# Performance work log

Measured on AMD Instinct MI355X. Metric: run time of the kernel, lower is better.

The kernel has to match this reference:

```python
import jax, jax.numpy as jnp
import numpy as np


def setup_inputs() -> dict:
    key = jax.random.key(0)
    k1, k2 = jax.random.split(key)
    B, S, D_IN, D_OUT = 4, 8192, 768, 768
    x = jax.random.normal(k1, (B, S, D_IN), dtype=jnp.float32)
    # kaiming_normal_(mode='fan_out', nonlinearity='linear') -> std = 1/sqrt(fan_out)
    weight = jax.random.normal(k2, (D_OUT, D_IN), dtype=jnp.float32) * (1.0 / jnp.sqrt(D_OUT))
    return {"x": x, "weight": weight}


def reference(x, weight):
    # Binarize weights with sign (0 -> 0, matching torch.sign), then F.linear:
    # out[..., o] = sum_i x[..., i] * sign(W)[o, i]
    w_bin = jnp.sign(weight)
    return jnp.einsum('bsi,oi->bso', x, w_bin)
```

## Files before the change

### kernel.cpp

```cpp
#include <hip/hip_runtime.h>
#include <hip/hip_bf16.h>

using f32x4 = __attribute__((ext_vector_type(4))) float;
using s16x8 = __attribute__((ext_vector_type(8))) short;

constexpr int KDIM = 768;
constexpr int NDIM = 768;
constexpr int BM = 128;
constexpr int BN = 128;
constexpr int BK = 32;
constexpr int NBN = NDIM / BN;
constexpr int NT = KDIM / BK;

__device__ __forceinline__ unsigned short f2bf(float f) {
    __bf16 h = (__bf16)f;
    return __builtin_bit_cast(unsigned short, h);
}

__device__ __forceinline__ short sgnbf(float w) {
    unsigned u = __builtin_bit_cast(unsigned, w);
    return (w != 0.f) ? (short)(unsigned short)(0x3F80u | ((u >> 16) & 0x8000u))
                      : (short)0;
}

__device__ __forceinline__ s16x8 cvt8(float4 u, float4 v) {
    s16x8 c;
    c[0] = (short)f2bf(u.x); c[1] = (short)f2bf(u.y);
    c[2] = (short)f2bf(u.z); c[3] = (short)f2bf(u.w);
    c[4] = (short)f2bf(v.x); c[5] = (short)f2bf(v.y);
    c[6] = (short)f2bf(v.z); c[7] = (short)f2bf(v.w);
    return c;
}

__global__ void binarize_w(const float* __restrict__ W, unsigned short* __restrict__ Wf) {
    const int g = blockIdx.x * 256 + threadIdx.x;
    const int lane = g & 63;
    const int grp  = g >> 6;
    const int n16l = grp & 7;
    const int bkt  = grp >> 3;
    const int bn   = bkt % NBN;
    const int kt   = bkt / NBN;
    const int col  = bn * 128 + n16l * 16 + (lane & 15);
    const int k0   = kt * 32 + (lane >> 4) * 8;
    const float* src = W + (size_t)col * KDIM + k0;
    s16x8 r;
    #pragma unroll
    for (int j = 0; j < 8; ++j) r[j] = sgnbf(src[j]);
    *(s16x8*)(Wf + (size_t)g * 8) = r;
}

#define BAR_NODRAIN() do {                                        \
    asm volatile("s_waitcnt lgkmcnt(0)" ::: "memory");            \
    __builtin_amdgcn_s_barrier();                                 \
    asm volatile("" ::: "memory");                                \
} while (0)

__device__ __forceinline__ int swzs(int s) { return s ^ (((s >> 4) & 3) << 2); }

template<bool PRE>
__global__ __launch_bounds__(256, 3)
void binlin_mfma(const float* __restrict__ X, const float* __restrict__ W,
                 const unsigned short* __restrict__ Wf, float* __restrict__ Out) {
    __shared__ __align__(16) unsigned short As[2][512 * 8];

    const int bid = blockIdx.x;
    const int cpx = gridDim.x >> 3;
    const int swz = (bid & 7) * cpx + (bid >> 3);
    const int bm = swz / NBN;
    const int bn = swz - bm * NBN;

    const int t    = threadIdx.x;
    const int lane = t & 63;
    const int wid  = t >> 6;
    const int wm   = (wid >> 1) * 64;
    const int wn   = (wid & 1) * 64;
    const int wm16 = (wid >> 1) * 4;
    const int wn16 = (wid & 1) * 4;

    const float* Xb = X + (size_t)bm * BM * KDIM;

    const int r   = t >> 2;
    const int c8  = (t & 3) * 8;
    const float* Abase = Xb + (size_t)r * KDIM + c8;
    const int sA1 = swzs((r >> 4) * 64 + (r & 15) + 16 * (t & 3));
    const int sA2 = swzs((r >> 4) * 64 + (r & 15) + 16 * (t & 3) + 256);

    auto loadA = [&](int kt, float4 a[4]) {
        const float* p = Abase + kt * BK;
        a[0] = *(const float4*)p;
        a[1] = *(const float4*)(p + 4);
        a[2] = *(const float4*)(p + (size_t)64 * KDIM);
        a[3] = *(const float4*)(p + (size_t)64 * KDIM + 4);
    };
    auto writeA = [&](int buf, float4 a[4]) {
        *(s16x8*)&As[buf][(size_t)sA1 * 8] = cvt8(a[0], a[1]);
        *(s16x8*)&As[buf][(size_t)sA2 * 8] = cvt8(a[2], a[3]);
    };
    auto loadB = [&](int kt, s16x8 b[4]) {
        if constexpr (PRE) {
            const unsigned short* q =
                Wf + ((size_t)(kt * NBN + bn) * 512 + wn16 * 64 + lane) * 8;
            #pragma unroll
            for (int n = 0; n < 4; ++n)
                b[n] = *(const s16x8*)(q + (size_t)n * 64 * 8);
        } else {
            #pragma unroll
            for (int n = 0; n < 4; ++n) {
                const int col = bn * 128 + (wn16 + n) * 16 + (lane & 15);
                const int k0  = kt * 32 + (lane >> 4) * 8;
                const float* wp = W + (size_t)col * KDIM + k0;
                float4 u = *(const float4*)wp;
                float4 v = *(const float4*)(wp + 4);
                s16x8 c;
                c[0] = sgnbf(u.x); c[1] = sgnbf(u.y); c[2] = sgnbf(u.z); c[3] = sgnbf(u.w);
                c[4] = sgnbf(v.x); c[5] = sgnbf(v.y); c[6] = sgnbf(v.z); c[7] = sgnbf(v.w);
                b[n] = c;
            }
        }
    };

    f32x4 acc[4][4] = {};
    float4 A0[4], A1[4];
    s16x8 B0[4], B1[4];

    loadA(0, A0);
    loadA(1, A1);
    loadB(0, B0);
    writeA(0, A0);
    BAR_NODRAIN();

    #pragma unroll
    for (int kt = 0; kt < NT; ++kt) {
        const int c = kt & 1;
        float4 (&AL)[4] = c ? A1 : A0;
        float4 (&AW)[4] = c ? A0 : A1;
        s16x8 (&BC)[4]  = c ? B1 : B0;
        s16x8 (&BL)[4]  = c ? B0 : B1;

        if (kt + 2 < NT) loadA(kt + 2, AL);
        if (kt + 1 < NT) loadB(kt + 1, BL);

        s16x8 af[4];
        #pragma unroll
        for (int m = 0; m < 4; ++m)
            af[m] = *(const s16x8*)&As[c][(size_t)swzs((wm16 + m) * 64 + lane) * 8];

        #pragma unroll
        for (int m = 0; m < 4; ++m)
            #pragma unroll
            for (int n = 0; n < 4; ++n)
                acc[m][n] = __builtin_amdgcn_mfma_f32_16x16x32_bf16(
                    af[m], BC[n], acc[m][n], 0, 0, 0);

        if (kt + 1 < NT) {
            writeA(c ^ 1, AW);
            BAR_NODRAIN();
        }
    }

    float* Ob = Out + (size_t)(bm * BM) * NDIM + bn * BN;
    const int lr = lane & 15;
    #pragma unroll
    for (int m = 0; m < 4; ++m) {
        const int row0 = wm + m * 16 + (lane >> 4) * 4;
        #pragma unroll
        for (int n = 0; n < 4; ++n) {
            const int col = wn + n * 16 + lr;
            #pragma unroll
            for (int rr = 0; rr < 4; ++rr)
                Ob[(size_t)(row0 + rr) * NDIM + col] = acc[m][n][rr];
        }
    }
}

extern "C" void kernel_launch(void* const* d_in, const int* in_sizes, int n_in,
                              void* d_out, int out_size, void* d_ws, size_t ws_size,
                              hipStream_t stream) {
    const float* X = (const float*)d_in[0];
    const float* W = (const float*)d_in[1];
    float* Out = (float*)d_out;
    const int M = in_sizes[0] / KDIM;
    const int grid = (M / BM) * NBN;
    const size_t need = (size_t)NDIM * KDIM * sizeof(unsigned short);

    if (ws_size >= need) {
        unsigned short* Wf = (unsigned short*)d_ws;
        binarize_w<<<(NT * NBN * 8 * 64) / 256, 256, 0, stream>>>(W, Wf);
        binlin_mfma<true><<<grid, 256, 0, stream>>>(X, W, Wf, Out);
    } else {
        binlin_mfma<false><<<grid, 256, 0, stream>>>(X, W, nullptr, Out);
    }
}
```

Before: 63.19 us.

## Enlarge tiles to 128x256x64 with 8 waves and phased barrier-interleaved MFMA schedule

Changes the block tile to BN=256, BK=64 with 512 threads (8 waves), and restructures the main loop into four phases per K step. Each phase interleaves the global loads and LDS writes with MFMA bursts, separated by barriers and s_setprio. The aim is to increase reuse per block, halve the number of K iterations, and overlap memory traffic with matrix work. The costs are more barriers per step, the loss of the LDS swizzle (risking bank conflicts), and lower occupancy from the larger register and LDS footprint.

```diff
diff --git a/kernel.cpp b/kernel.cpp
--- a/kernel.cpp
+++ b/kernel.cpp
@@ -7,8 +7,8 @@
 constexpr int KDIM = 768;
 constexpr int NDIM = 768;
 constexpr int BM = 128;
-constexpr int BN = 128;
-constexpr int BK = 32;
+constexpr int BN = 256;
+constexpr int BK = 64;
 constexpr int NBN = NDIM / BN;
 constexpr int NT = KDIM / BK;
 
@@ -34,14 +34,16 @@
 
 __global__ void binarize_w(const float* __restrict__ W, unsigned short* __restrict__ Wf) {
     const int g = blockIdx.x * 256 + threadIdx.x;
-    const int lane = g & 63;
-    const int grp  = g >> 6;
-    const int n16l = grp & 7;
-    const int bkt  = grp >> 3;
-    const int bn   = bkt % NBN;
-    const int kt   = bkt / NBN;
-    const int col  = bn * 128 + n16l * 16 + (lane & 15);
-    const int k0   = kt * 32 + (lane >> 4) * 8;
+    const int lane  = g & 63;
+    const int sg    = g >> 6;
+    const int srow  = sg & 31;
+    const int chunk = sg >> 5;
+    const int bn = chunk % NBN;
+    const int kt = chunk / NBN;
+    const int kk  = srow >> 4;
+    const int n16 = srow & 15;
+    const int col = bn * 256 + n16 * 16 + (lane & 15);
+    const int k0  = kt * 64 + kk * 32 + (lane >> 4) * 8;
     const float* src = W + (size_t)col * KDIM + k0;
     s16x8 r;
     #pragma unroll
@@ -49,19 +51,37 @@
     *(s16x8*)(Wf + (size_t)g * 8) = r;
 }
 
-#define BAR_NODRAIN() do {                                        \
-    asm volatile("s_waitcnt lgkmcnt(0)" ::: "memory");            \
-    __builtin_amdgcn_s_barrier();                                 \
-    asm volatile("" ::: "memory");                                \
+#define PHASE(C, KK, MB, BARR, ...) do {                                       \
+    s16x8 af0_ = *(const s16x8*)&As[C][(size_t)(((KK)*8 + wr4 + (MB)) * 64 + lane) * 8];       \
+    s16x8 af1_ = *(const s16x8*)&As[C][(size_t)(((KK)*8 + wr4 + (MB) + 1) * 64 + lane) * 8];   \
+    __VA_ARGS__;                                                               \
+    __builtin_amdgcn_s_barrier();                                              \
+    __builtin_amdgcn_s_setprio(1);                                             \
+    _Pragma("unroll")                                                          \
+    for (int n_ = 0; n_ < 4; ++n_) {                                           \
+        acc[MB][n_]     = __builtin_amdgcn_mfma_f32_16x16x32_bf16(af0_, BARR[KK][n_], acc[MB][n_], 0, 0, 0);       \
+        acc[(MB)+1][n_] = __builtin_amdgcn_mfma_f32_16x16x32_bf16(af1_, BARR[KK][n_], acc[(MB)+1][n_], 0, 0, 0);   \
+    }                                                                          \
+    __builtin_amdgcn_s_setprio(0);                                             \
+    __builtin_amdgcn_s_barrier();                                              \
 } while (0)
 
-__device__ __forceinline__ int swzs(int s) { return s ^ (((s >> 4) & 3) << 2); }
+#define KSTEP(C, BCUR, BNXT, KT, PF) do {                                      \
+    PHASE(C, 0, 0, BCUR, { if (PF) loadA((KT) + 1, aR); });                    \
+    PHASE(C, 0, 2, BCUR, { if (PF) loadB((KT) + 1, BNXT); });                  \
+    PHASE(C, 1, 0, BCUR, {});                                                  \
+    PHASE(C, 1, 2, BCUR, {                                                     \
+        if (PF) writeA((C) ^ 1, aR);                                           \
+        asm volatile("s_waitcnt lgkmcnt(0)" ::: "memory");                     \
+        __builtin_amdgcn_sched_barrier(0);                                     \
+    });                                                                        \
+} while (0)
 
 template<bool PRE>
-__global__ __launch_bounds__(256, 3)
+__global__ __launch_bounds__(512, 2)
 void binlin_mfma(const float* __restrict__ X, const float* __restrict__ W,
                  const unsigned short* __restrict__ Wf, float* __restrict__ Out) {
-    __shared__ __align__(16) unsigned short As[2][512 * 8];
+    __shared__ __align__(16) unsigned short As[2][1024 * 8];
 
     const int bid = blockIdx.x;
     const int cpx = gridDim.x >> 3;
@@ -72,93 +92,76 @@
     const int t    = threadIdx.x;
     const int lane = t & 63;
     const int wid  = t >> 6;
-    const int wm   = (wid >> 1) * 64;
-    const int wn   = (wid & 1) * 64;
-    const int wm16 = (wid >> 1) * 4;
-    const int wn16 = (wid & 1) * 4;
+    const int wr   = wid >> 2;
+    const int wc   = wid & 3;
+    const int wm   = wr * 64;
+    const int wn   = wc * 64;
+    const int wr4  = wr * 4;
 
     const float* Xb = X + (size_t)bm * BM * KDIM;
 
-    const int r   = t >> 2;
-    const int c8  = (t & 3) * 8;
-    const float* Abase = Xb + (size_t)r * KDIM + c8;
-    const int sA1 = swzs((r >> 4) * 64 + (r & 15) + 16 * (t & 3));
-    const int sA2 = swzs((r >> 4) * 64 + (r & 15) + 16 * (t & 3) + 256);
+    const int r  = t >> 2;
+    const int q  = t & 3;
+    const float* Abase = Xb + (size_t)r * KDIM + q * 8;
+    const int sA0 = ((r >> 4)) * 64 + (r & 15) + 16 * q;
+    const int sA1 = (8 + (r >> 4)) * 64 + (r & 15) + 16 * q;
 
+    float4 aR[4];
     auto loadA = [&](int kt, float4 a[4]) {
         const float* p = Abase + kt * BK;
         a[0] = *(const float4*)p;
         a[1] = *(const float4*)(p + 4);
-        a[2] = *(const float4*)(p + (size_t)64 * KDIM);
-        a[3] = *(const float4*)(p + (size_t)64 * KDIM + 4);
+        a[2] = *(const float4*)(p + 32);
+        a[3] = *(const float4*)(p + 36);
     };
     auto writeA = [&](int buf, float4 a[4]) {
-        *(s16x8*)&As[buf][(size_t)sA1 * 8] = cvt8(a[0], a[1]);
-        *(s16x8*)&As[buf][(size_t)sA2 * 8] = cvt8(a[2], a[3]);
+        *(s16x8*)&As[buf][(size_t)sA0 * 8] = cvt8(a[0], a[1]);
+        *(s16x8*)&As[buf][(size_t)sA1 * 8] = cvt8(a[2], a[3]);
     };
-    auto loadB = [&](int kt, s16x8 b[4]) {
+    auto loadB = [&](int kt, s16x8 b[2][4]) {
         if constexpr (PRE) {
-            const unsigned short* q =
-                Wf + ((size_t)(kt * NBN + bn) * 512 + wn16 * 64 + lane) * 8;
+            const unsigned short* base = Wf + (size_t)(kt * NBN + bn) * 2048 * 8;
             #pragma unroll
-            for (int n = 0; n < 4; ++n)
-                b[n] = *(const s16x8*)(q + (size_t)n * 64 * 8);
+            for (int kk = 0; kk < 2; ++kk)
+                #pragma unroll
+                for (int n = 0; n < 4; ++n)
+                    b[kk][n] = *(const s16x8*)(base + (size_t)((kk * 16 + wc * 4 + n) * 64 + lane) * 8);
         } else {
             #pragma unroll
-            for (int n = 0; n < 4; ++n) {
-                const int col = bn * 128 + (wn16 + n) * 16 + (lane & 15);
-                const int k0  = kt * 32 + (lane >> 4) * 8;
-                const float* wp = W + (size_t)col * KDIM + k0;
-                float4 u = *(const float4*)wp;
-                float4 v = *(const float4*)(wp + 4);
-                s16x8 c;
-                c[0] = sgnbf(u.x); c[1] = sgnbf(u.y); c[2] = sgnbf(u.z); c[3] = sgnbf(u.w);
-                c[4] = sgnbf(v.x); c[5] = sgnbf(v.y); c[6] = sgnbf(v.z); c[7] = sgnbf(v.w);
-                b[n] = c;
-            }
+            for (int kk = 0; kk < 2; ++kk)
+                #pragma unroll
+                for (int n = 0; n < 4; ++n) {
+                    const int col = bn * 256 + (wc * 4 + n) * 16 + (lane & 15);
+                    const int k0  = kt * 64 + kk * 32 + (lane >> 4) * 8;
+                    const float* wp = W + (size_t)col * KDIM + k0;
+                    float4 u = *(const float4*)wp;
+                    float4 v = *(const float4*)(wp + 4);
+                    s16x8 c;
+                    c[0] = sgnbf(u.x); c[1] = sgnbf(u.y); c[2] = sgnbf(u.z); c[3] = sgnbf(u.w);
+                    c[4] = sgnbf(v.x); c[5] = sgnbf(v.y); c[6] = sgnbf(v.z); c[7] = sgnbf(v.w);
+                    b[kk][n] = c;
+                }
         }
     };
 
     f32x4 acc[4][4] = {};
-    float4 A0[4], A1[4];
-    s16x8 B0[4], B1[4];
+    s16x8 B0[2][4], B1[2][4];
 
-    loadA(0, A0);
-    loadA(1, A1);
+    loadA(0, aR);
+    writeA(0, aR);
     loadB(0, B0);
-    writeA(0, A0);
-    BAR_NODRAIN();
+    asm volatile("s_waitcnt lgkmcnt(0)" ::: "memory");
+    __builtin_amdgcn_s_barrier();
 
-    #pragma unroll
-    for (int kt = 0; kt < NT; ++kt) {
-        const int c = kt & 1;
-        float4 (&AL)[4] = c ? A1 : A0;
-        float4 (&AW)[4] = c ? A0 : A1;
-        s16x8 (&BC)[4]  = c ? B1 : B0;
-        s16x8 (&BL)[4]  = c ? B0 : B1;
+    for (int kt2 = 0; kt2 < 5; ++kt2) {
+        const int kt = 2 * kt2;
+        KSTEP(0, B0, B1, kt, true);
+        KSTEP(1, B1, B0, kt + 1, true);
+    }
+    KSTEP(0, B0, B1, 10, true);
+    KSTEP(1, B1, B0, 11, false);
 
-        if (kt + 2 < NT) loadA(kt + 2, AL);
-        if (kt + 1 < NT) loadB(kt + 1, BL);
-
-        s16x8 af[4];
-        #pragma unroll
-        for (int m = 0; m < 4; ++m)
-            af[m] = *(const s16x8*)&As[c][(size_t)swzs((wm16 + m) * 64 + lane) * 8];
-
-        #pragma unroll
-        for (int m = 0; m < 4; ++m)
-            #pragma unroll
-            for (int n = 0; n < 4; ++n)
-                acc[m][n] = __builtin_amdgcn_mfma_f32_16x16x32_bf16(
-                    af[m], BC[n], acc[m][n], 0, 0, 0);
-
-        if (kt + 1 < NT) {
-            writeA(c ^ 1, AW);
-            BAR_NODRAIN();
-        }
-    }
-
-    float* Ob = Out + (size_t)(bm * BM) * NDIM + bn * BN;
+    float* Ob = Out + (size_t)(bm * BM) * NDIM + (size_t)bn * BN;
     const int lr = lane & 15;
     #pragma unroll
     for (int m = 0; m < 4; ++m) {
@@ -185,9 +188,9 @@
 
     if (ws_size >= need) {
         unsigned short* Wf = (unsigned short*)d_ws;
-        binarize_w<<<(NT * NBN * 8 * 64) / 256, 256, 0, stream>>>(W, Wf);
-        binlin_mfma<true><<<grid, 256, 0, stream>>>(X, W, Wf, Out);
+        binarize_w<<<(NT * NBN * 2048) / 256, 256, 0, stream>>>(W, Wf);
+        binlin_mfma<true><<<grid, 512, 0, stream>>>(X, W, Wf, Out);
     } else {
-        binlin_mfma<false><<<grid, 256, 0, stream>>>(X, W, nullptr, Out);
+        binlin_mfma<false><<<grid, 512, 0, stream>>>(X, W, nullptr, Out);
     }
 }
```

New measurement: 85.07 us. 34.6% more time.
